# Kernel optimization log

Measured on AMD Instinct MI355X. Metric: run time of the kernel, lower is better.

The kernel has to match this reference:

```python
import jax, jax.numpy as jnp
import numpy as np

N_NODES = 100000
IN_FEATS = 64
H_FEATS = 64
N_PARTS = 16
N_EDGES = 1200000


def setup_inputs() -> dict:
    key = jax.random.key(0)
    ks = jax.random.split(key, 12)
    features = jax.random.normal(ks[0], (N_NODES, IN_FEATS), dtype=jnp.float32)
    src = jax.random.randint(ks[1], (N_EDGES,), 0, N_NODES, dtype=jnp.int64)
    dst = jax.random.randint(ks[2], (N_EDGES,), 0, N_NODES, dtype=jnp.int64)
    s_in = 1.0 / np.sqrt(IN_FEATS)
    s_h = 1.0 / np.sqrt(H_FEATS)
    W_self1 = jax.random.normal(ks[3], (IN_FEATS, H_FEATS), dtype=jnp.float32) * s_in
    W_neigh1 = jax.random.normal(ks[4], (IN_FEATS, H_FEATS), dtype=jnp.float32) * s_in
    b1 = jnp.zeros((H_FEATS,), dtype=jnp.float32)
    W_self2 = jax.random.normal(ks[5], (H_FEATS, H_FEATS), dtype=jnp.float32) * s_h
    W_neigh2 = jax.random.normal(ks[6], (H_FEATS, H_FEATS), dtype=jnp.float32) * s_h
    b2 = jnp.zeros((H_FEATS,), dtype=jnp.float32)
    W_fc = jax.random.normal(ks[7], (H_FEATS, N_PARTS), dtype=jnp.float32) * s_h
    b_fc = jnp.zeros((N_PARTS,), dtype=jnp.float32)
    return {"features": features, "src": src, "dst": dst,
            "W_self1": W_self1, "W_neigh1": W_neigh1, "b1": b1,
            "W_self2": W_self2, "W_neigh2": W_neigh2, "b2": b2,
            "W_fc": W_fc, "b_fc": b_fc}


def reference(features, src, dst, W_self1, W_neigh1, b1, W_self2, W_neigh2, b2, W_fc, b_fc):
    N = features.shape[0]
    # in-degree per destination node (mean aggregator; zero-degree nodes stay 0)
    ones = jnp.ones(src.shape[0], dtype=features.dtype)
    deg = jax.ops.segment_sum(ones, dst, num_segments=N)
    inv_deg = jnp.where(deg > 0, 1.0 / jnp.maximum(deg, 1.0), 0.0)[:, None]

    def sage_mean(x, W_self, W_neigh, b):
        # gather source features along edges, mean-aggregate at destinations
        agg = jax.ops.segment_sum(x[src], dst, num_segments=N) * inv_deg
        return x @ W_self + agg @ W_neigh + b

    h = jax.nn.relu(sage_mean(features, W_self1, W_neigh1, b1))
    h = jax.nn.relu(sage_mean(h, W_self2, W_neigh2, b2))
    logits = h @ W_fc + b_fc
    return jax.nn.softmax(logits, axis=1)
```

## Files before the change

kernel.cpp:

```cpp
#include <hip/hip_runtime.h>
#include <math.h>

#define F 64
#define NP 16
#define BK_SHIFT 9
#define BK_SIZE 512
#define MAXB 256
#define CHUNK 8192
#define CAP 8192

typedef __bf16 bf16x8 __attribute__((ext_vector_type(8)));
typedef float f32x4 __attribute__((ext_vector_type(4)));

__device__ __forceinline__ short f2bf(float v) {
    union { __bf16 b; short s; } u; u.b = (__bf16)v; return u.s;
}
__device__ __forceinline__ float bfbits2f(short s) {
    union { short s; __bf16 b; } u; u.s = s; return (float)u.b;
}
__device__ __forceinline__ float bf2f(unsigned short u) {
    union { unsigned u; float f; } t; t.u = ((unsigned)u) << 16; return t.f;
}

__global__ __launch_bounds__(1024) void k_bucket_tobf(
    const int* __restrict__ src, const int* __restrict__ dst,
    int* __restrict__ bcur, unsigned* __restrict__ ebuf, int nE, int nChunk,
    const float* __restrict__ fin, unsigned short* __restrict__ fout, int nF)
{
    int t = threadIdx.x;
    if ((int)blockIdx.x >= nChunk) {
        int i = ((blockIdx.x - nChunk) * 1024 + t) * 4;
        if (i < nF) {
            float4 v = *(const float4*)(fin + i);
            short4 r;
            r.x = f2bf(v.x); r.y = f2bf(v.y); r.z = f2bf(v.z); r.w = f2bf(v.w);
            *(short4*)(fout + i) = r;
        }
        return;
    }
    __shared__ int h[MAXB];
    __shared__ int base[MAXB];
    int lo = blockIdx.x * CHUNK, hi = min(lo + CHUNK, nE);
    int s[8], d[8];
#pragma unroll
    for (int k = 0; k < 8; ++k) {
        int i = lo + t + k * 1024;
        if (i < hi) { s[k] = src[i]; d[k] = dst[i]; } else { d[k] = -1; }
    }
    for (int i = t; i < MAXB; i += 1024) h[i] = 0;
    __syncthreads();
#pragma unroll
    for (int k = 0; k < 8; ++k)
        if (d[k] >= 0) atomicAdd(&h[d[k] >> BK_SHIFT], 1);
    __syncthreads();
    for (int i = t; i < MAXB; i += 1024) {
        base[i] = h[i] ? (i * CAP + atomicAdd(&bcur[i], h[i])) : 0;
        h[i] = 0;
    }
    __syncthreads();
#pragma unroll
    for (int k = 0; k < 8; ++k)
        if (d[k] >= 0) {
            int b = d[k] >> BK_SHIFT;
            int r = atomicAdd(&h[b], 1);
            ebuf[base[b] + r] = (unsigned)s[k] | ((unsigned)(d[k] & (BK_SIZE - 1)) << 17);
        }
}

__global__ __launch_bounds__(BK_SIZE) void k_bcsr(const unsigned* __restrict__ ebuf,
                                                  const int* __restrict__ bcur,
                                                  int* __restrict__ rowstart,
                                                  int* __restrict__ deg,
                                                  int* __restrict__ csr,
                                                  float* __restrict__ invd, int nN) {
    __shared__ int cnt[BK_SIZE];
    __shared__ int sc[BK_SIZE];
    __shared__ int cur[BK_SIZE];
    int b = blockIdx.x, t = threadIdx.x;
    int nodeBase = b << BK_SHIFT;
    int ebase = b * CAP;
    int ecnt = bcur[b];
    cnt[t] = 0; __syncthreads();
    for (int i = t; i < ecnt; i += BK_SIZE)
        atomicAdd(&cnt[ebuf[ebase + i] >> 17], 1);
    __syncthreads();
    int c = cnt[t];
    sc[t] = c; __syncthreads();
    for (int off = 1; off < BK_SIZE; off <<= 1) {
        int u = (t >= off) ? sc[t - off] : 0;
        __syncthreads();
        sc[t] += u;
        __syncthreads();
    }
    int ex = sc[t] - c;
    cur[t] = ex;
    int node = nodeBase + t;
    if (node < nN) {
        rowstart[node] = ebase + ex;
        deg[node] = c;
        invd[node] = c ? 1.0f / (float)c : 0.0f;
    }
    __syncthreads();
    for (int i = t; i < ecnt; i += BK_SIZE) {
        unsigned e = ebuf[ebase + i];
        int r = atomicAdd(&cur[e >> 17], 1);
        csr[ebase + r] = (int)(e & 0x1FFFFu);
    }
}

__global__ __launch_bounds__(256) void k_gather(
    const unsigned short* __restrict__ xb, const int* __restrict__ csr,
    const int* __restrict__ rowstart, const int* __restrict__ deg,
    const float* __restrict__ invd, unsigned short* __restrict__ aggb, int nN)
{
    int wid = (blockIdx.x * blockDim.x + threadIdx.x) >> 6;
    int lane = threadIdx.x & 63;
    int g = lane >> 4, c = lane & 15;
    int g16 = g * 16;
#define ROW(s) (const ushort4*)(xb + (size_t)(unsigned)(s) * F + c * 4)
#define ACC(v) { ax += bf2f((v).x); ay += bf2f((v).y); az += bf2f((v).z); aw += bf2f((v).w); }
    int n = wid * 4 + g;
    bool valid = (n < nN);
    int rs = 0, dg = 0;
    if (valid) { rs = rowstart[n]; dg = deg[n]; }
    int e0 = (valid && c < dg)      ? csr[rs + c]      : 0;
    int e1 = (valid && 16 + c < dg) ? csr[rs + 16 + c] : 0;
    float ax = 0.f, ay = 0.f, az = 0.f, aw = 0.f;
    int d1 = min(dg, 16);
    int j = 0;
    for (; j + 4 <= d1; j += 4) {
        int s0 = __shfl(e0, g16 + j);
        int s1 = __shfl(e0, g16 + j + 1);
        int s2 = __shfl(e0, g16 + j + 2);
        int s3 = __shfl(e0, g16 + j + 3);
        ushort4 v0 = *ROW(s0); ushort4 v1 = *ROW(s1);
        ushort4 v2 = *ROW(s2); ushort4 v3 = *ROW(s3);
        ACC(v0); ACC(v1); ACC(v2); ACC(v3);
    }
    for (; j < d1; ++j) {
        int s0 = __shfl(e0, g16 + j);
        ushort4 v0 = *ROW(s0);
        ACC(v0);
    }
    if (dg > 16) {
        int d2 = min(dg, 32);
        for (j = 16; j + 2 <= d2; j += 2) {
            int s0 = __shfl(e1, g16 + j - 16);
            int s1 = __shfl(e1, g16 + j - 15);
            ushort4 v0 = *ROW(s0); ushort4 v1 = *ROW(s1);
            ACC(v0); ACC(v1);
        }
        for (; j < d2; ++j) {
            int s0 = __shfl(e1, g16 + j - 16);
            ushort4 v0 = *ROW(s0);
            ACC(v0);
        }
        for (j = 32; j < dg; ++j) {
            int s0 = csr[rs + j];
            ushort4 v0 = *ROW(s0);
            ACC(v0);
        }
    }
    if (valid) {
        float iv = invd[n];
        short4 r;
        r.x = f2bf(ax * iv); r.y = f2bf(ay * iv);
        r.z = f2bf(az * iv); r.w = f2bf(aw * iv);
        *(short4*)(aggb + (size_t)n * F + c * 4) = r;
    }
#undef ROW
#undef ACC
}

template<bool DO_FC, bool XBF>
__global__ __launch_bounds__(256) void k_layer(
    const float* __restrict__ xf,
    const unsigned short* __restrict__ xhi, const unsigned short* __restrict__ xlo,
    const unsigned short* __restrict__ aggb,
    const float* __restrict__ Ws, const float* __restrict__ Wn,
    const float* __restrict__ bias,
    const float* __restrict__ Wfc, const float* __restrict__ bfc,
    unsigned short* __restrict__ outhi, unsigned short* __restrict__ outlo,
    float* __restrict__ out, int nN)
{
    __shared__ short lds_hi[16][136];
    __shared__ short lds_lo[16][72];
    __shared__ short lds_hb[16][72];

    int t = threadIdx.x;
    int w = t >> 6, l = t & 63;
    int base = blockIdx.x * 16;

    {
        int r = t >> 4, c4 = t & 15;
        int node = base + r;
        if (XBF) {
            short4 hx = make_short4(0, 0, 0, 0), lx = make_short4(0, 0, 0, 0);
            if (node < nN) {
                hx = *(const short4*)(xhi + (size_t)node * F + c4 * 4);
                lx = *(const short4*)(xlo + (size_t)node * F + c4 * 4);
            }
            *(short4*)&lds_hi[r][c4 * 4] = hx;
            *(short4*)&lds_lo[r][c4 * 4] = lx;
        } else {
            float4 xv = make_float4(0.f, 0.f, 0.f, 0.f);
            if (node < nN) xv = *(const float4*)(xf + (size_t)node * F + c4 * 4);
            const float* xp = &xv.x;
            short hx[4], lx[4];
#pragma unroll
            for (int jj = 0; jj < 4; ++jj) {
                float v = xp[jj]; short h = f2bf(v);
                hx[jj] = h; lx[jj] = f2bf(v - bfbits2f(h));
            }
            *(short4*)&lds_hi[r][c4 * 4] = make_short4(hx[0], hx[1], hx[2], hx[3]);
            *(short4*)&lds_lo[r][c4 * 4] = make_short4(lx[0], lx[1], lx[2], lx[3]);
        }
        short4 av = make_short4(0, 0, 0, 0);
        if (node < nN) av = *(const short4*)(aggb + (size_t)node * F + c4 * 4);
        *(short4*)&lds_hi[r][64 + c4 * 4] = av;
    }

    int kg = l >> 4;
    int col = w * 16 + (l & 15);
    bf16x8 bw[4];
#pragma unroll
    for (int kt = 0; kt < 4; ++kt)
#pragma unroll
        for (int e = 0; e < 8; ++e) {
            int k = kt * 32 + kg * 8 + e;
            float wv = (k < F) ? Ws[k * F + col] : Wn[(k - F) * F + col];
            bw[kt][e] = (__bf16)wv;
        }

    __syncthreads();

    int m = l & 15;
    f32x4 acc = {0.f, 0.f, 0.f, 0.f};
#pragma unroll
    for (int kt = 0; kt < 4; ++kt) {
        bf16x8 ah = *(const bf16x8*)&lds_hi[m][kt * 32 + kg * 8];
        acc = __builtin_amdgcn_mfma_f32_16x16x32_bf16(ah, bw[kt], acc, 0, 0, 0);
        if (kt < 2) {
            bf16x8 al = *(const bf16x8*)&lds_lo[m][kt * 32 + kg * 8];
            acc = __builtin_amdgcn_mfma_f32_16x16x32_bf16(al, bw[kt], acc, 0, 0, 0);
        }
    }

    float bj = bias[col];
    if constexpr (!DO_FC) {
#pragma unroll
        for (int i = 0; i < 4; ++i) {
            int node = base + (l >> 4) * 4 + i;
            if (node < nN) {
                float v = fmaxf(acc[i] + bj, 0.f);
                short h = f2bf(v);
                outhi[(size_t)node * F + col] = (unsigned short)h;
                outlo[(size_t)node * F + col] = (unsigned short)f2bf(v - bfbits2f(h));
            }
        }
    } else {
#pragma unroll
        for (int i = 0; i < 4; ++i) {
            int nit = (l >> 4) * 4 + i;
            lds_hb[nit][col] = f2bf(fmaxf(acc[i] + bj, 0.f));
        }
        __syncthreads();
        if (w == 0) {
            bf16x8 wf[2];
#pragma unroll
            for (int kt = 0; kt < 2; ++kt)
#pragma unroll
                for (int e = 0; e < 8; ++e) {
                    int k = kt * 32 + kg * 8 + e;
                    wf[kt][e] = (__bf16)Wfc[k * NP + (l & 15)];
                }
            f32x4 lacc = {0.f, 0.f, 0.f, 0.f};
#pragma unroll
            for (int kt = 0; kt < 2; ++kt) {
                bf16x8 hfrag = *(const bf16x8*)&lds_hb[m][kt * 32 + kg * 8];
                lacc = __builtin_amdgcn_mfma_f32_16x16x32_bf16(hfrag, wf[kt], lacc, 0, 0, 0);
            }
            float bf = bfc[l & 15];
#pragma unroll
            for (int i = 0; i < 4; ++i) {
                float lg = lacc[i] + bf;
                float mm = lg;
                for (int off = 8; off; off >>= 1) mm = fmaxf(mm, __shfl_xor(mm, off, 16));
                float e2 = __expf(lg - mm);
                float ss = e2;
                for (int off = 8; off; off >>= 1) ss += __shfl_xor(ss, off, 16);
                int node = base + (l >> 4) * 4 + i;
                if (node < nN) out[(size_t)node * NP + (l & 15)] = e2 / ss;
            }
        }
    }
}

extern "C" void kernel_launch(void* const* d_in, const int* in_sizes, int n_in,
                              void* d_out, int out_size, void* d_ws, size_t ws_size,
                              hipStream_t stream) {
    const float* features = (const float*)d_in[0];
    const int*   src      = (const int*)d_in[1];
    const int*   dst      = (const int*)d_in[2];
    const float* Ws1      = (const float*)d_in[3];
    const float* Wn1      = (const float*)d_in[4];
    const float* b1       = (const float*)d_in[5];
    const float* Ws2      = (const float*)d_in[6];
    const float* Wn2      = (const float*)d_in[7];
    const float* b2       = (const float*)d_in[8];
    const float* Wfc      = (const float*)d_in[9];
    const float* bfc      = (const float*)d_in[10];
    float* out = (float*)d_out;

    int nE = in_sizes[1];
    int nN = in_sizes[0] / F;
    int nB = (nN + BK_SIZE - 1) >> BK_SHIFT;
    int nTiles = (nN + 15) / 16;
    int nChunk = (nE + CHUNK - 1) / CHUNK;
    int nTobf = (nN * F / 4 + 1023) / 1024;

    unsigned* ebuf  = (unsigned*)d_ws;
    int*   bcur     = (int*)(ebuf + (size_t)nB * CAP);
    int*   rowstart = bcur + MAXB;
    int*   deg      = rowstart + nN;
    int*   csr      = deg + nN;
    float* invd     = (float*)(csr + (size_t)nB * CAP);
    unsigned short* xhi  = (unsigned short*)(invd + nN);
    unsigned short* zhi  = xhi + (size_t)nN * F;
    unsigned short* zlo  = zhi + (size_t)nN * F;
    unsigned short* aggb = zlo + (size_t)nN * F;

    hipMemsetAsync(bcur, 0, MAXB * sizeof(int), stream);

    k_bucket_tobf<<<nChunk + nTobf, 1024, 0, stream>>>(
        src, dst, bcur, ebuf, nE, nChunk, features, xhi, nN * F);
    k_bcsr<<<nB, BK_SIZE, 0, stream>>>(ebuf, bcur, rowstart, deg, csr, invd, nN);

    k_gather<<<nTiles, 256, 0, stream>>>(xhi, csr, rowstart, deg, invd, aggb, nN);
    k_layer<false, false><<<nTiles, 256, 0, stream>>>(
        features, nullptr, nullptr, aggb, Ws1, Wn1, b1, nullptr, nullptr,
        zhi, zlo, nullptr, nN);

    k_gather<<<nTiles, 256, 0, stream>>>(zhi, csr, rowstart, deg, invd, aggb, nN);
    k_layer<true, true><<<nTiles, 256, 0, stream>>>(
        nullptr, zhi, zlo, aggb, Ws2, Wn2, b2, Wfc, bfc,
        nullptr, nullptr, out, nN);
}
```

Measured before the change: 121.9 us.

## Widen gather to 8 lanes per node and drop bf16 low-part split for layer-2 input

The gather kernel now gives each node 8 lanes that each load 16 bytes (8 bf16 values), so one wave handles 8 nodes and each row fetch uses wider vector loads. The layer-1 output is stored only as a single bf16 array instead of a hi/lo bf16 pair. This removes one output write stream, one input read stream and the low-part MFMAs in layer 2. The cost is lower precision for the hidden activations of layer 2, which may push results closer to the tolerance limit.

```diff
diff --git a/kernel.cpp b/kernel.cpp
--- a/kernel.cpp
+++ b/kernel.cpp
@@ -11,6 +11,7 @@
 
 typedef __bf16 bf16x8 __attribute__((ext_vector_type(8)));
 typedef float f32x4 __attribute__((ext_vector_type(4)));
+typedef unsigned short u16x8 __attribute__((ext_vector_type(8)));
 
 __device__ __forceinline__ short f2bf(float v) {
     union { __bf16 b; short s; } u; u.b = (__bf16)v; return u.s;
@@ -115,73 +116,70 @@
 {
     int wid = (blockIdx.x * blockDim.x + threadIdx.x) >> 6;
     int lane = threadIdx.x & 63;
-    int g = lane >> 4, c = lane & 15;
-    int g16 = g * 16;
-#define ROW(s) (const ushort4*)(xb + (size_t)(unsigned)(s) * F + c * 4)
-#define ACC(v) { ax += bf2f((v).x); ay += bf2f((v).y); az += bf2f((v).z); aw += bf2f((v).w); }
-    int n = wid * 4 + g;
+    int g = lane >> 3, c = lane & 7;
+    int g8 = g * 8;
+    int n = wid * 8 + g;
     bool valid = (n < nN);
     int rs = 0, dg = 0;
     if (valid) { rs = rowstart[n]; dg = deg[n]; }
     int e0 = (valid && c < dg)      ? csr[rs + c]      : 0;
-    int e1 = (valid && 16 + c < dg) ? csr[rs + 16 + c] : 0;
-    float ax = 0.f, ay = 0.f, az = 0.f, aw = 0.f;
-    int d1 = min(dg, 16);
-    int j = 0;
-    for (; j + 4 <= d1; j += 4) {
-        int s0 = __shfl(e0, g16 + j);
-        int s1 = __shfl(e0, g16 + j + 1);
-        int s2 = __shfl(e0, g16 + j + 2);
-        int s3 = __shfl(e0, g16 + j + 3);
-        ushort4 v0 = *ROW(s0); ushort4 v1 = *ROW(s1);
-        ushort4 v2 = *ROW(s2); ushort4 v3 = *ROW(s3);
-        ACC(v0); ACC(v1); ACC(v2); ACC(v3);
-    }
-    for (; j < d1; ++j) {
-        int s0 = __shfl(e0, g16 + j);
-        ushort4 v0 = *ROW(s0);
-        ACC(v0);
-    }
-    if (dg > 16) {
-        int d2 = min(dg, 32);
-        for (j = 16; j + 2 <= d2; j += 2) {
-            int s0 = __shfl(e1, g16 + j - 16);
-            int s1 = __shfl(e1, g16 + j - 15);
-            ushort4 v0 = *ROW(s0); ushort4 v1 = *ROW(s1);
-            ACC(v0); ACC(v1);
-        }
-        for (; j < d2; ++j) {
-            int s0 = __shfl(e1, g16 + j - 16);
-            ushort4 v0 = *ROW(s0);
+    int e1 = (valid && 8 + c < dg)  ? csr[rs + 8 + c]  : 0;
+    int e2 = (valid && 16 + c < dg) ? csr[rs + 16 + c] : 0;
+    int e3 = (valid && 24 + c < dg) ? csr[rs + 24 + c] : 0;
+    float a0 = 0.f, a1 = 0.f, a2 = 0.f, a3 = 0.f, a4 = 0.f, a5 = 0.f, a6 = 0.f, a7 = 0.f;
+#define LOADROW(sv) (*(const u16x8*)(xb + (size_t)(unsigned)(sv) * F + c * 8))
+#define ACC(v) { a0 += bf2f((v)[0]); a1 += bf2f((v)[1]); a2 += bf2f((v)[2]); a3 += bf2f((v)[3]); \
+                 a4 += bf2f((v)[4]); a5 += bf2f((v)[5]); a6 += bf2f((v)[6]); a7 += bf2f((v)[7]); }
+#define SEG(eR, base8, dcap) { \
+        int dend = min(dg, dcap); \
+        int j = base8; \
+        for (; j + 4 <= dend; j += 4) { \
+            int s0 = __shfl(eR, g8 + j - base8); \
+            int s1 = __shfl(eR, g8 + j - base8 + 1); \
+            int s2 = __shfl(eR, g8 + j - base8 + 2); \
+            int s3 = __shfl(eR, g8 + j - base8 + 3); \
+            u16x8 v0 = LOADROW(s0); u16x8 v1 = LOADROW(s1); \
+            u16x8 v2 = LOADROW(s2); u16x8 v3 = LOADROW(s3); \
+            ACC(v0); ACC(v1); ACC(v2); ACC(v3); \
+        } \
+        for (; j < dend; ++j) { \
+            int s0 = __shfl(eR, g8 + j - base8); \
+            u16x8 v0 = LOADROW(s0); \
+            ACC(v0); \
+        } }
+    SEG(e0, 0, 8);
+    if (dg > 8)  SEG(e1, 8, 16);
+    if (dg > 16) SEG(e2, 16, 24);
+    if (dg > 24) SEG(e3, 24, 32);
+    if (dg > 32) {
+        for (int j = 32; j < dg; ++j) {
+            int s0 = csr[rs + j];
+            u16x8 v0 = LOADROW(s0);
             ACC(v0);
         }
-        for (j = 32; j < dg; ++j) {
-            int s0 = csr[rs + j];
-            ushort4 v0 = *ROW(s0);
-            ACC(v0);
-        }
-    }
+    }
+#undef SEG
+#undef ACC
+#undef LOADROW
     if (valid) {
         float iv = invd[n];
-        short4 r;
-        r.x = f2bf(ax * iv); r.y = f2bf(ay * iv);
-        r.z = f2bf(az * iv); r.w = f2bf(aw * iv);
-        *(short4*)(aggb + (size_t)n * F + c * 4) = r;
-    }
-#undef ROW
-#undef ACC
+        u16x8 r;
+        r[0] = (unsigned short)f2bf(a0 * iv); r[1] = (unsigned short)f2bf(a1 * iv);
+        r[2] = (unsigned short)f2bf(a2 * iv); r[3] = (unsigned short)f2bf(a3 * iv);
+        r[4] = (unsigned short)f2bf(a4 * iv); r[5] = (unsigned short)f2bf(a5 * iv);
+        r[6] = (unsigned short)f2bf(a6 * iv); r[7] = (unsigned short)f2bf(a7 * iv);
+        *(u16x8*)(aggb + (size_t)n * F + c * 8) = r;
+    }
 }
 
 template<bool DO_FC, bool XBF>
 __global__ __launch_bounds__(256) void k_layer(
-    const float* __restrict__ xf,
-    const unsigned short* __restrict__ xhi, const unsigned short* __restrict__ xlo,
+    const float* __restrict__ xf, const unsigned short* __restrict__ xhi,
     const unsigned short* __restrict__ aggb,
     const float* __restrict__ Ws, const float* __restrict__ Wn,
     const float* __restrict__ bias,
     const float* __restrict__ Wfc, const float* __restrict__ bfc,
-    unsigned short* __restrict__ outhi, unsigned short* __restrict__ outlo,
-    float* __restrict__ out, int nN)
+    unsigned short* __restrict__ outhi, float* __restrict__ out, int nN)
 {
     __shared__ short lds_hi[16][136];
     __shared__ short lds_lo[16][72];
@@ -195,13 +193,9 @@
         int r = t >> 4, c4 = t & 15;
         int node = base + r;
         if (XBF) {
-            short4 hx = make_short4(0, 0, 0, 0), lx = make_short4(0, 0, 0, 0);
-            if (node < nN) {
-                hx = *(const short4*)(xhi + (size_t)node * F + c4 * 4);
-                lx = *(const short4*)(xlo + (size_t)node * F + c4 * 4);
-            }
+            short4 hx = make_short4(0, 0, 0, 0);
+            if (node < nN) hx = *(const short4*)(xhi + (size_t)node * F + c4 * 4);
             *(short4*)&lds_hi[r][c4 * 4] = hx;
-            *(short4*)&lds_lo[r][c4 * 4] = lx;
         } else {
             float4 xv = make_float4(0.f, 0.f, 0.f, 0.f);
             if (node < nN) xv = *(const float4*)(xf + (size_t)node * F + c4 * 4);
@@ -240,7 +234,7 @@
     for (int kt = 0; kt < 4; ++kt) {
         bf16x8 ah = *(const bf16x8*)&lds_hi[m][kt * 32 + kg * 8];
         acc = __builtin_amdgcn_mfma_f32_16x16x32_bf16(ah, bw[kt], acc, 0, 0, 0);
-        if (kt < 2) {
+        if (!XBF && kt < 2) {
             bf16x8 al = *(const bf16x8*)&lds_lo[m][kt * 32 + kg * 8];
             acc = __builtin_amdgcn_mfma_f32_16x16x32_bf16(al, bw[kt], acc, 0, 0, 0);
         }
@@ -253,9 +247,7 @@
             int node = base + (l >> 4) * 4 + i;
             if (node < nN) {
                 float v = fmaxf(acc[i] + bj, 0.f);
-                short h = f2bf(v);
-                outhi[(size_t)node * F + col] = (unsigned short)h;
-                outlo[(size_t)node * F + col] = (unsigned short)f2bf(v - bfbits2f(h));
+                outhi[(size_t)node * F + col] = (unsigned short)f2bf(v);
             }
         }
     } else {
@@ -316,6 +308,7 @@
     int nN = in_sizes[0] / F;
     int nB = (nN + BK_SIZE - 1) >> BK_SHIFT;
     int nTiles = (nN + 15) / 16;
+    int nG = (nN + 31) / 32;
     int nChunk = (nE + CHUNK - 1) / CHUNK;
     int nTobf = (nN * F / 4 + 1023) / 1024;
 
@@ -327,8 +320,7 @@
     float* invd     = (float*)(csr + (size_t)nB * CAP);
     unsigned short* xhi  = (unsigned short*)(invd + nN);
     unsigned short* zhi  = xhi + (size_t)nN * F;
-    unsigned short* zlo  = zhi + (size_t)nN * F;
-    unsigned short* aggb = zlo + (size_t)nN * F;
+    unsigned short* aggb = zhi + (size_t)nN * F;
 
     hipMemsetAsync(bcur, 0, MAXB * sizeof(int), stream);
 
@@ -336,13 +328,11 @@
         src, dst, bcur, ebuf, nE, nChunk, features, xhi, nN * F);
     k_bcsr<<<nB, BK_SIZE, 0, stream>>>(ebuf, bcur, rowstart, deg, csr, invd, nN);
 
-    k_gather<<<nTiles, 256, 0, stream>>>(xhi, csr, rowstart, deg, invd, aggb, nN);
+    k_gather<<<nG, 256, 0, stream>>>(xhi, csr, rowstart, deg, invd, aggb, nN);
     k_layer<false, false><<<nTiles, 256, 0, stream>>>(
-        features, nullptr, nullptr, aggb, Ws1, Wn1, b1, nullptr, nullptr,
-        zhi, zlo, nullptr, nN);
-
-    k_gather<<<nTiles, 256, 0, stream>>>(zhi, csr, rowstart, deg, invd, aggb, nN);
+        features, nullptr, aggb, Ws1, Wn1, b1, nullptr, nullptr, zhi, nullptr, nN);
+
+    k_gather<<<nG, 256, 0, stream>>>(zhi, csr, rowstart, deg, invd, aggb, nN);
     k_layer<true, true><<<nTiles, 256, 0, stream>>>(
-        nullptr, zhi, zlo, aggb, Ws2, Wn2, b2, Wfc, bfc,
-        nullptr, nullptr, out, nN);
-}
+        nullptr, zhi, aggb, Ws2, Wn2, b2, Wfc, bfc, nullptr, out, nN);
+}
```

Measured after the change: 117.4 us, median of 2. 1.04x faster.
